# Kernel optimization log

Hardware: AMD Instinct MI355X
Metric: run time of the kernel (lower is better)

## Reference

```python
import jax, jax.numpy as jnp
import numpy as np

HID = 4096; H = 128; P = 64; N = 128; G = 8; K = 4; CH = 128
INTER = H * P                      # 8192
CONV_DIM = INTER + 2 * G * N       # 10240
PROJ = INTER + CONV_DIM + H        # 18560
EPS = 1e-5


def segsum(x):
    # stable segment-sum: out[..., i, j] = sum_{j < k <= i} x[..., k]; -inf above diagonal
    T = x.shape[-1]
    xe = jnp.repeat(x[..., None], T, axis=-1)          # [..., i, j] = x[..., i]
    strict = jnp.tril(jnp.ones((T, T), bool), -1)
    s = jnp.cumsum(jnp.where(strict, xe, 0.0), axis=-2)
    keep = jnp.tril(jnp.ones((T, T), bool), 0)
    return jnp.where(keep, s, -jnp.inf)


def setup_inputs() -> dict:
    key = jax.random.key(0)
    ks = jax.random.split(key, 6)
    b, L = 2, 2048
    hidden_states = jax.random.normal(ks[0], (b, L, HID), jnp.float32)
    in_proj_w = jax.random.normal(ks[1], (PROJ, HID), jnp.float32) * (HID ** -0.5)
    conv_w = jax.random.normal(ks[2], (CONV_DIM, 1, K), jnp.float32) * 0.2
    conv_b = jax.random.normal(ks[3], (CONV_DIM,), jnp.float32) * 0.02
    dt_bias = jnp.ones((H,), jnp.float32)
    A_log = jnp.log(jnp.arange(1, H + 1, dtype=jnp.float32))
    D = jnp.ones((H,), jnp.float32)
    norm_weight = jnp.ones((INTER,), jnp.float32)
    out_proj_w = jax.random.normal(ks[4], (HID, INTER), jnp.float32) * (INTER ** -0.5)
    return dict(hidden_states=hidden_states, in_proj_w=in_proj_w, conv_w=conv_w, conv_b=conv_b,
                dt_bias=dt_bias, A_log=A_log, D=D, norm_weight=norm_weight, out_proj_w=out_proj_w)


def _mamba2(hidden_states, in_proj_w, conv_w, conv_b, dt_bias, A_log, D, norm_weight, out_proj_w):
    b, L, _ = hidden_states.shape
    nchunk = L // CH  # seq_len chosen to be a multiple of chunk_size (pad_size = 0)

    # in_proj and split into gate | conv path (x,B,C) | dt
    proj = hidden_states @ in_proj_w.T
    gate, hBC, dt = jnp.split(proj, [INTER, INTER + CONV_DIM], axis=-1)

    # causal depthwise conv1d (padding k-1, truncate) + SiLU
    xp = jnp.pad(hBC.transpose(0, 2, 1), ((0, 0), (0, 0), (K - 1, 0)))
    xc = jax.lax.conv_general_dilated(xp, conv_w, (1,), 'VALID',
                                      feature_group_count=CONV_DIM,
                                      dimension_numbers=('NCW', 'OIW', 'NCW'))
    hBC = jax.nn.silu((xc + conv_b[None, :, None]).transpose(0, 2, 1))
    hs, Bx, Cx = jnp.split(hBC, [INTER, INTER + G * N], axis=-1)

    A = -jnp.exp(A_log)                      # [H]
    dt = jax.nn.softplus(dt + dt_bias)       # time_step_limit = (0, inf) -> clamp is no-op

    hs = hs.reshape(b, L, H, P)
    rep = H // G
    Bm = jnp.tile(Bx.reshape(b, L, G, N), (1, 1, rep, 1))   # matches torch .repeat
    Cm = jnp.tile(Cx.reshape(b, L, G, N), (1, 1, rep, 1))

    D_res = D[None, None, :, None] * hs      # [b,L,H,P]

    # discretize and chunk
    X = (hs * dt[..., None]).reshape(b, nchunk, CH, H, P)
    A_dt = (A[None, None, :] * dt).reshape(b, nchunk, CH, H).transpose(0, 3, 1, 2)  # [b,H,c,l]
    Bc = Bm.reshape(b, nchunk, CH, H, N)
    Cc = Cm.reshape(b, nchunk, CH, H, N)
    A_cs = jnp.cumsum(A_dt, axis=-1)

    # 1. intra-chunk (diagonal blocks)
    Lmat = jnp.exp(segsum(A_dt))                              # [b,H,c,l,s]
    Gm = jnp.einsum('bclhn,bcshn->bclsh', Cc, Bc)
    M = Gm * Lmat.transpose(0, 2, 3, 4, 1)                    # [b,c,l,s,H]
    Y_diag = jnp.einsum('bclsh,bcshp->bclhp', M, X)

    # 2. per-chunk states
    decay_states = jnp.exp(A_cs[..., -1:] - A_cs)             # [b,H,c,l]
    B_decay = Bc * decay_states.transpose(0, 2, 3, 1)[..., None]
    states = jnp.einsum('bclhn,bclhp->bchpn', B_decay, X)     # [b,c,H,P,N]

    # 3. inter-chunk recurrence
    states = jnp.concatenate([jnp.zeros_like(states[:, :1]), states], axis=1)
    A_last = jnp.pad(A_cs[..., -1], ((0, 0), (0, 0), (1, 0)))  # [b,H,c+1]
    decay_chunk = jnp.exp(segsum(A_last)).transpose(0, 3, 2, 1)  # [b,c+1,c+1,H]
    new_states = jnp.einsum('bzjh,bzhpn->bjhpn', decay_chunk, states)
    prev_states = new_states[:, :-1]                           # [b,c,H,P,N]

    # 4. state -> output
    sdo = jnp.exp(A_cs).transpose(0, 2, 3, 1)                  # [b,c,l,H]
    Y_off = jnp.einsum('bclhn,bchpn->bclhp', Cc, prev_states) * sdo[..., None]

    y = (Y_diag + Y_off).reshape(b, L, H, P) + D_res
    scan_out = y.reshape(b, L, INTER)

    # gated group RMSNorm (norm_before_gate=False: gate first, then group-RMS)
    xg = scan_out * jax.nn.silu(gate)
    xr = xg.reshape(b, L, G, INTER // G)
    xr = xr * jax.lax.rsqrt(jnp.mean(xr * xr, axis=-1, keepdims=True) + EPS)
    normed = xr.reshape(b, L, INTER) * norm_weight

    return normed @ out_proj_w.T


def reference(hidden_states, in_proj_w, conv_w, conv_b, dt_bias, A_log, D, norm_weight, out_proj_w):
    return _mamba2(hidden_states, in_proj_w, conv_w, conv_b, dt_bias, A_log, D, norm_weight, out_proj_w)
```

## Files before the change

### kernel.cpp

```cpp
#include <hip/hip_runtime.h>

#define NH 128
#define PD 64
#define NSD 128
#define NG 8
#define CHK 128
#define HIDD 4096
#define INTER_D 8192
#define CONV_D 10240
#define PROJ_D 18560
#define NPAD 18688
#define SEQ 2048
#define ROWS 4096
#define NCH 16

typedef __attribute__((ext_vector_type(8))) short bf16x8;
typedef __attribute__((ext_vector_type(4))) float f32x4;

__device__ __forceinline__ unsigned short f2bf(float f) {
  unsigned int u = __float_as_uint(f);
  u += 0x7FFF + ((u >> 16) & 1);
  return (unsigned short)(u >> 16);
}
__device__ __forceinline__ float bf2f(unsigned short s) {
  return __uint_as_float(((unsigned int)s) << 16);
}

__device__ __forceinline__ void gld16(const unsigned short* g, unsigned short* l) {
  __builtin_amdgcn_global_load_lds(
      (__attribute__((address_space(1))) const void*)g,
      (__attribute__((address_space(3))) void*)l, 16, 0, 0);
}

#define BAR() __builtin_amdgcn_s_barrier()
#define SCHED() __builtin_amdgcn_sched_barrier(0)
#define VMCNT(n) asm volatile("s_waitcnt vmcnt(" #n ")" ::: "memory")

__device__ __forceinline__ bf16x8 ldsfrag(const unsigned short* slot, int row, int kslot) {
  int byte = row * 128 + (((kslot ^ (row & 7)) << 4));
  return *(const bf16x8*)((const char*)slot + byte);
}

__global__ __launch_bounds__(256) void cvt_kernel(const float* __restrict__ in,
                                                  unsigned short* __restrict__ out,
                                                  size_t n) {
  size_t i = ((size_t)blockIdx.x * 256 + threadIdx.x) * 4;
  if (i < n) {
    float4 f = *(const float4*)(in + i);
    ushort4 o;
    o.x = f2bf(f.x); o.y = f2bf(f.y); o.z = f2bf(f.z); o.w = f2bf(f.w);
    *(ushort4*)(out + i) = o;
  }
}

template <int OUT_BF16>
__global__ __launch_bounds__(512, 2) void gemm256(const unsigned short* __restrict__ A,
                                                  const unsigned short* __restrict__ B,
                                                  unsigned short* __restrict__ outb,
                                                  float* __restrict__ outf,
                                                  int Nreal, int K) {
  __shared__ unsigned short lds[8][8192];
  int tid = threadIdx.x, l = tid & 63, w = tid >> 6;
  int wm = w >> 2, wn = w & 3;
  int il = l & 15, fog = l >> 4;
  int bid = blockIdx.x;
  int xcd = bid & 7, local = bid >> 3;
  int mt = xcd * 2 + (local & 1), nt = local >> 1;
  const unsigned short* Abase = A + (size_t)mt * 256 * K;
  const unsigned short* Bbase = B + (size_t)nt * 256 * K;
  int NT = K >> 6;

  f32x4 acc[2][2][4][2];
#pragma unroll
  for (int a = 0; a < 2; ++a)
#pragma unroll
    for (int b = 0; b < 2; ++b)
#pragma unroll
      for (int m = 0; m < 4; ++m)
#pragma unroll
        for (int n = 0; n < 2; ++n) acc[a][b][m][n] = (f32x4){0.f, 0.f, 0.f, 0.f};

  auto STG = [&](int tt, int ty) {
    int tc = tt < NT ? tt : NT - 1;
    const unsigned short* g = ((ty & 1) ? Bbase : Abase) + (size_t)((ty >> 1) * 128) * K + tc * 64;
    unsigned short* sp = (unsigned short*)lds[(tt & 1) * 4 + ty];
#pragma unroll
    for (int j = 0; j < 2; ++j) {
      int row = (j * 8 + w) * 8 + (l >> 3);
      int scol = ((l & 7) ^ (row & 7)) * 8;
      gld16(g + (size_t)row * K + scol, sp + (j * 8 + w) * 512);
    }
  };

#define LDA(SLOT)                                          \
  _Pragma("unroll") for (int mi = 0; mi < 4; ++mi)         \
  _Pragma("unroll") for (int kk = 0; kk < 2; ++kk)         \
      av[mi][kk] = ldsfrag(SLOT, wm * 64 + mi * 16 + il, kk * 4 + fog);
#define LDB(QN, SLOT)                                      \
  _Pragma("unroll") for (int ni = 0; ni < 2; ++ni)         \
  _Pragma("unroll") for (int kk = 0; kk < 2; ++kk)         \
      bv[QN][ni][kk] = ldsfrag(SLOT, wn * 32 + ni * 16 + il, kk * 4 + fog);
#define MFMA_PH(QM, QN)                                    \
  _Pragma("unroll") for (int mi = 0; mi < 4; ++mi)         \
  _Pragma("unroll") for (int ni = 0; ni < 2; ++ni)         \
  _Pragma("unroll") for (int kk = 0; kk < 2; ++kk)         \
      acc[QM][QN][mi][ni] = __builtin_amdgcn_mfma_f32_16x16x32_bf16( \
          av[mi][kk], bv[QN][ni][kk], acc[QM][QN][mi][ni], 0, 0, 0);

  STG(0, 0); STG(0, 1); STG(0, 3); STG(0, 2);
  VMCNT(2);
  BAR(); SCHED();

  for (int t = 0; t < NT; ++t) {
    const unsigned short* sA0 = lds[(t & 1) * 4 + 0];
    const unsigned short* sB0 = lds[(t & 1) * 4 + 1];
    const unsigned short* sA1 = lds[(t & 1) * 4 + 2];
    const unsigned short* sB1 = lds[(t & 1) * 4 + 3];
    bf16x8 av[4][2], bv[2][2][2];
    LDA(sA0); LDB(0, sB0); LDB(1, sB1);
    STG(t + 1, 0); STG(t + 1, 1);
    BAR();
    __builtin_amdgcn_s_setprio(1);
    MFMA_PH(0, 0);
    __builtin_amdgcn_s_setprio(0);
    VMCNT(4);
    BAR(); SCHED();
    STG(t + 1, 3);
    __builtin_amdgcn_s_setprio(1);
    MFMA_PH(0, 1);
    __builtin_amdgcn_s_setprio(0);
    BAR();
    LDA(sA1);
    STG(t + 1, 2);
    BAR();
    __builtin_amdgcn_s_setprio(1);
    MFMA_PH(1, 0);
    __builtin_amdgcn_s_setprio(0);
    BAR();
    __builtin_amdgcn_s_setprio(1);
    MFMA_PH(1, 1);
    __builtin_amdgcn_s_setprio(0);
    VMCNT(2);
    BAR(); SCHED();
  }

  int rl = (l >> 4) * 4;
#pragma unroll
  for (int qm = 0; qm < 2; ++qm)
#pragma unroll
    for (int qn = 0; qn < 2; ++qn)
#pragma unroll
      for (int mi = 0; mi < 4; ++mi)
#pragma unroll
        for (int ni = 0; ni < 2; ++ni) {
          int grow = mt * 256 + qm * 128 + wm * 64 + mi * 16 + rl;
          int gcol = nt * 256 + qn * 128 + wn * 32 + ni * 16 + il;
          if (!OUT_BF16 || gcol < Nreal) {
#pragma unroll
            for (int r = 0; r < 4; ++r) {
              float v = acc[qm][qn][mi][ni][r];
              if (OUT_BF16)
                outb[(size_t)(grow + r) * Nreal + gcol] = f2bf(v);
              else
                outf[(size_t)(grow + r) * Nreal + gcol] = v;
            }
          }
        }
#undef LDA
#undef LDB
#undef MFMA_PH
}

__global__ __launch_bounds__(128) void dts_kernel(const unsigned short* __restrict__ proj,
                                                  const float* __restrict__ dt_bias,
                                                  const float* __restrict__ A_log,
                                                  float* __restrict__ dtg,
                                                  float* __restrict__ acsg) {
  int bc = blockIdx.x;
  int h = threadIdx.x;
  int b = bc >> 4, c = bc & 15;
  float A = -__expf(A_log[h]);
  float bias = dt_bias[h];
  float cum = 0.f;
  int row0 = b * SEQ + c * CHK;
  for (int ll = 0; ll < CHK; ++ll) {
    float x = bf2f(proj[(size_t)(row0 + ll) * PROJ_D + (PROJ_D - NH) + h]) + bias;
    float d = (x > 20.f) ? x : log1pf(expf(x));
    dtg[(size_t)(row0 + ll) * NH + h] = d;
    cum += A * d;
    acsg[(((size_t)bc * NH) + h) * CHK + ll] = cum;
  }
}

__global__ __launch_bounds__(256) void conv_kernel(const unsigned short* __restrict__ proj,
                                                   const float* __restrict__ cw,
                                                   const float* __restrict__ cb,
                                                   unsigned short* __restrict__ xbc) {
  int ch = blockIdx.x * 256 + threadIdx.x;
  int row = blockIdx.y;
  int b = row >> 11, ll = row & 2047;
  float acc = cb[ch];
#pragma unroll
  for (int k = 0; k < 4; ++k) {
    int l2 = ll - 3 + k;
    if (l2 >= 0)
      acc += bf2f(proj[(size_t)(b * SEQ + l2) * PROJ_D + INTER_D + ch]) * cw[ch * 4 + k];
  }
  float s = acc / (1.f + __expf(-acc));
  xbc[(size_t)row * CONV_D + ch] = f2bf(s);
}

__global__ __launch_bounds__(512) void e1a_kernel(const unsigned short* __restrict__ xbc,
                                                  const float* __restrict__ dtg,
                                                  const float* __restrict__ acsg,
                                                  float* __restrict__ yb) {
  int bid = blockIdx.x;
  int h = bid & 127, c = (bid >> 7) & 15, b = bid >> 11;
  int g = h & 7;
  int row0 = b * SEQ + c * CHK;
  __shared__ __align__(16) char smem[53248];
  unsigned short* Cst = (unsigned short*)smem;
  unsigned short* Bst = (unsigned short*)(smem + 10240);
  unsigned short* Mt = (unsigned short*)smem;
  unsigned short* XT = (unsigned short*)(smem + 34816);
  float* Acs = (float*)(smem + 52224);
  int tid = threadIdx.x, lane = tid & 63, wv = tid >> 6;
  int fo = (lane >> 4) * 8, il = lane & 15, rl = (lane >> 4) * 4;
  if (tid < 128) Acs[tid] = acsg[(((size_t)(b * NCH + c) * NH) + h) * CHK + tid];

  f32x4 gm[8];
#pragma unroll
  for (int i = 0; i < 8; ++i) gm[i] = (f32x4){0.f, 0.f, 0.f, 0.f};
  int srow = tid >> 2, scol = (tid & 3) * 8;
  for (int kc = 0; kc < 4; ++kc) {
    __syncthreads();
    *(int4*)(Cst + srow * 40 + scol) =
        *(const int4*)(xbc + (size_t)(row0 + srow) * CONV_D + INTER_D + NG * NSD + g * NSD + kc * 32 + scol);
    *(int4*)(Bst + srow * 40 + scol) =
        *(const int4*)(xbc + (size_t)(row0 + srow) * CONV_D + INTER_D + g * NSD + kc * 32 + scol);
    __syncthreads();
    bf16x8 a = *(const bf16x8*)&Cst[(wv * 16 + il) * 40 + fo];
#pragma unroll
    for (int ni = 0; ni < 8; ++ni) {
      bf16x8 bb = *(const bf16x8*)&Bst[(ni * 16 + il) * 40 + fo];
      gm[ni] = __builtin_amdgcn_mfma_f32_16x16x32_bf16(a, bb, gm[ni], 0, 0, 0);
    }
  }
  __syncthreads();
#pragma unroll
  for (int ni = 0; ni < 8; ++ni) {
    int s = ni * 16 + il;
#pragma unroll
    for (int r = 0; r < 4; ++r) {
      int ll = wv * 16 + rl + r;
      float v = (s <= ll) ? gm[ni][r] * __expf(Acs[ll] - Acs[s]) : 0.f;
      Mt[ll * 136 + s] = f2bf(v);
    }
  }
#pragma unroll
  for (int j = 0; j < 2; ++j) {
    int q = tid + j * 512;
    int ll = q >> 3, p0 = (q & 7) * 8;
    int row = row0 + ll;
    float dtv = dtg[(size_t)row * NH + h];
    int4 raw = *(const int4*)(xbc + (size_t)row * CONV_D + h * PD + p0);
    unsigned short* u = (unsigned short*)&raw;
#pragma unroll
    for (int e = 0; e < 8; ++e) XT[(p0 + e) * 136 + ll] = f2bf(bf2f(u[e]) * dtv);
  }
  __syncthreads();
  f32x4 yd[4];
#pragma unroll
  for (int i = 0; i < 4; ++i) yd[i] = (f32x4){0.f, 0.f, 0.f, 0.f};
#pragma unroll
  for (int ks = 0; ks < 4; ++ks) {
    bf16x8 a = *(const bf16x8*)&Mt[(wv * 16 + il) * 136 + ks * 32 + fo];
#pragma unroll
    for (int pi = 0; pi < 4; ++pi) {
      bf16x8 bb = *(const bf16x8*)&XT[(pi * 16 + il) * 136 + ks * 32 + fo];
      yd[pi] = __builtin_amdgcn_mfma_f32_16x16x32_bf16(a, bb, yd[pi], 0, 0, 0);
    }
  }
#pragma unroll
  for (int pi = 0; pi < 4; ++pi) {
    int p = pi * 16 + il;
#pragma unroll
    for (int r = 0; r < 4; ++r) {
      int ll = wv * 16 + rl + r;
      yb[(size_t)(row0 + ll) * INTER_D + h * PD + p] = yd[pi][r];
    }
  }
}

__global__ __launch_bounds__(256) void e1b_kernel(const unsigned short* __restrict__ xbc,
                                                  const float* __restrict__ dtg,
                                                  const float* __restrict__ acsg,
                                                  float* __restrict__ states) {
  int bid = blockIdx.x;
  int h = bid & 127, c = (bid >> 7) & 15, b = bid >> 11;
  int g = h & 7;
  int row0 = b * SEQ + c * CHK;
  __shared__ __align__(16) char smem[52736];
  unsigned short* XT = (unsigned short*)smem;
  unsigned short* BdT = (unsigned short*)(smem + 17408);
  float* Acs = (float*)(smem + 52224);
  int tid = threadIdx.x, lane = tid & 63, wv = tid >> 6;
  int fo = (lane >> 4) * 8, il = lane & 15, rl = (lane >> 4) * 4;
  if (tid < 128) Acs[tid] = acsg[(((size_t)(b * NCH + c) * NH) + h) * CHK + tid];
  __syncthreads();
#pragma unroll
  for (int j = 0; j < 4; ++j) {
    int q = tid + j * 256;
    int ll = q >> 3, p0 = (q & 7) * 8;
    int row = row0 + ll;
    float dtv = dtg[(size_t)row * NH + h];
    int4 raw = *(const int4*)(xbc + (size_t)row * CONV_D + h * PD + p0);
    unsigned short* u = (unsigned short*)&raw;
#pragma unroll
    for (int e = 0; e < 8; ++e) XT[(p0 + e) * 136 + ll] = f2bf(bf2f(u[e]) * dtv);
  }
#pragma unroll
  for (int j = 0; j < 8; ++j) {
    int q = tid + j * 256;
    int ll = q >> 4, n0 = (q & 15) * 8;
    float dec = __expf(Acs[CHK - 1] - Acs[ll]);
    int4 raw = *(const int4*)(xbc + (size_t)(row0 + ll) * CONV_D + INTER_D + g * NSD + n0);
    unsigned short* u = (unsigned short*)&raw;
#pragma unroll
    for (int e = 0; e < 8; ++e) BdT[(n0 + e) * 136 + ll] = f2bf(bf2f(u[e]) * dec);
  }
  __syncthreads();
  f32x4 st[8];
#pragma unroll
  for (int i = 0; i < 8; ++i) st[i] = (f32x4){0.f, 0.f, 0.f, 0.f};
#pragma unroll
  for (int ks = 0; ks < 4; ++ks) {
    bf16x8 a = *(const bf16x8*)&XT[(wv * 16 + il) * 136 + ks * 32 + fo];
#pragma unroll
    for (int ni = 0; ni < 8; ++ni) {
      bf16x8 bb = *(const bf16x8*)&BdT[(ni * 16 + il) * 136 + ks * 32 + fo];
      st[ni] = __builtin_amdgcn_mfma_f32_16x16x32_bf16(a, bb, st[ni], 0, 0, 0);
    }
  }
  size_t base = ((size_t)(b * NH + h) * NCH + c) * (PD * NSD);
#pragma unroll
  for (int ni = 0; ni < 8; ++ni) {
    int n = ni * 16 + il;
#pragma unroll
    for (int r = 0; r < 4; ++r) {
      int p = wv * 16 + rl + r;
      states[base + p * NSD + n] = st[ni][r];
    }
  }
}

__global__ __launch_bounds__(256) void e2_kernel(const float* __restrict__ acsg,
                                                 float* __restrict__ states) {
  int bh = blockIdx.x;
  int b = bh >> 7, h = bh & 127;
  int t = threadIdx.x;
  float S[32];
#pragma unroll
  for (int j = 0; j < 32; ++j) S[j] = 0.f;
  for (int c = 0; c < NCH; ++c) {
    float alast = acsg[(((size_t)(b * NCH + c) * NH) + h) * CHK + (CHK - 1)];
    float dec = __expf(alast);
    size_t base = ((size_t)bh * NCH + c) * (PD * NSD);
#pragma unroll
    for (int j = 0; j < 32; ++j) {
      size_t e = base + (size_t)j * 256 + t;
      float v = states[e];
      states[e] = S[j];
      S[j] = S[j] * dec + v;
    }
  }
}

__global__ __launch_bounds__(256) void e3_kernel(const unsigned short* __restrict__ xbc,
                                                 const float* __restrict__ acsg,
                                                 const float* __restrict__ states,
                                                 float* __restrict__ yb) {
  int bid = blockIdx.x;
  int h = bid & 127, c = (bid >> 7) & 15, b = bid >> 11;
  int g = h & 7;
  int row0 = b * SEQ + c * CHK;
  __shared__ __align__(16) char smem[52736];
  unsigned short* Ct = (unsigned short*)smem;
  unsigned short* Sp = (unsigned short*)(smem + 34816);
  float* Acs = (float*)(smem + 52224);
  int tid = threadIdx.x, lane = tid & 63, wv = tid >> 6;
  int fo = (lane >> 4) * 8, il = lane & 15, rl = (lane >> 4) * 4;
  if (tid < 128) Acs[tid] = acsg[(((size_t)(b * NCH + c) * NH) + h) * CHK + tid];
  size_t sbase = ((size_t)(b * NH + h) * NCH + c) * (PD * NSD);
#pragma unroll
  for (int j = 0; j < 8; ++j) {
    int q = tid + j * 256;
    int ll = q >> 4, n0 = (q & 15) * 8;
    *(int4*)(Ct + ll * 136 + n0) =
        *(const int4*)(xbc + (size_t)(row0 + ll) * CONV_D + INTER_D + NG * NSD + g * NSD + n0);
  }
#pragma unroll
  for (int j = 0; j < 4; ++j) {
    int q = tid + j * 256;
    int p = q >> 4, n0 = (q & 15) * 8;
    unsigned short tmp[8];
#pragma unroll
    for (int e = 0; e < 8; ++e) tmp[e] = f2bf(states[sbase + p * NSD + n0 + e]);
    *(int4*)(Sp + p * 136 + n0) = *(int4*)tmp;
  }
  __syncthreads();
  f32x4 yo[2][4];
#pragma unroll
  for (int i = 0; i < 2; ++i)
#pragma unroll
    for (int j = 0; j < 4; ++j) yo[i][j] = (f32x4){0.f, 0.f, 0.f, 0.f};
#pragma unroll
  for (int ks = 0; ks < 4; ++ks) {
    bf16x8 a0 = *(const bf16x8*)&Ct[(wv * 32 + il) * 136 + ks * 32 + fo];
    bf16x8 a1 = *(const bf16x8*)&Ct[(wv * 32 + 16 + il) * 136 + ks * 32 + fo];
#pragma unroll
    for (int pi = 0; pi < 4; ++pi) {
      bf16x8 bb = *(const bf16x8*)&Sp[(pi * 16 + il) * 136 + ks * 32 + fo];
      yo[0][pi] = __builtin_amdgcn_mfma_f32_16x16x32_bf16(a0, bb, yo[0][pi], 0, 0, 0);
      yo[1][pi] = __builtin_amdgcn_mfma_f32_16x16x32_bf16(a1, bb, yo[1][pi], 0, 0, 0);
    }
  }
#pragma unroll
  for (int mi = 0; mi < 2; ++mi)
#pragma unroll
    for (int pi = 0; pi < 4; ++pi)
#pragma unroll
      for (int r = 0; r < 4; ++r) {
        int ll = wv * 32 + mi * 16 + rl + r;
        int p = pi * 16 + il;
        size_t idx = (size_t)(row0 + ll) * INTER_D + h * PD + p;
        yb[idx] += yo[mi][pi][r] * __expf(Acs[ll]);
      }
}

__global__ __launch_bounds__(256) void fnorm_kernel(const float* __restrict__ yb,
                                                    const unsigned short* __restrict__ xbc,
                                                    const unsigned short* __restrict__ proj,
                                                    const float* __restrict__ Dp,
                                                    const float* __restrict__ nw,
                                                    unsigned short* __restrict__ normed) {
  int row = blockIdx.x >> 3;
  int gg = blockIdx.x & 7;
  int t = threadIdx.x;
  float v[4];
  float ss = 0.f;
#pragma unroll
  for (int j = 0; j < 4; ++j) {
    int ch = gg * 1024 + j * 256 + t;
    int h = ch >> 6;
    float yy = yb[(size_t)row * INTER_D + ch];
    float hs = bf2f(xbc[(size_t)row * CONV_D + ch]);
    float gt = bf2f(proj[(size_t)row * PROJ_D + ch]);
    float val = yy + Dp[h] * hs;
    val *= gt / (1.f + __expf(-gt));
    v[j] = val;
    ss += val * val;
  }
  __shared__ float sred[256];
  sred[t] = ss;
  __syncthreads();
  for (int ofs = 128; ofs > 0; ofs >>= 1) {
    if (t < ofs) sred[t] += sred[t + ofs];
    __syncthreads();
  }
  float rms = rsqrtf(sred[0] / 1024.f + 1e-5f);
#pragma unroll
  for (int j = 0; j < 4; ++j) {
    int ch = gg * 1024 + j * 256 + t;
    normed[(size_t)row * INTER_D + ch] = f2bf(v[j] * rms * nw[ch]);
  }
}

extern "C" void kernel_launch(void* const* d_in, const int* in_sizes, int n_in,
                              void* d_out, int out_size, void* d_ws, size_t ws_size,
                              hipStream_t stream) {
  (void)in_sizes; (void)n_in; (void)out_size; (void)ws_size;
  const float* hs = (const float*)d_in[0];
  const float* w1 = (const float*)d_in[1];
  const float* cw = (const float*)d_in[2];
  const float* cb = (const float*)d_in[3];
  const float* dtb = (const float*)d_in[4];
  const float* alog = (const float*)d_in[5];
  const float* Dp = (const float*)d_in[6];
  const float* nw = (const float*)d_in[7];
  const float* w2 = (const float*)d_in[8];
  float* out = (float*)d_out;
  char* ws = (char*)d_ws;

  unsigned short* hsb = (unsigned short*)(ws);
  unsigned short* w1b = (unsigned short*)(ws + 33554432);
  unsigned short* w2b = (unsigned short*)(ws + 186646528);
  unsigned short* proj = (unsigned short*)(ws + 253755392);
  unsigned short* xbc = (unsigned short*)(ws + 405798912);
  float* dtg = (float*)(ws + 489684992);
  float* acsg = (float*)(ws + 491782144);
  float* states = (float*)(ws + 493879296);
  float* yb = (float*)(ws + 628097024);
  unsigned short* normed = (unsigned short*)(ws);

  cvt_kernel<<<dim3(16384), dim3(256), 0, stream>>>(hs, hsb, (size_t)ROWS * HIDD);
  cvt_kernel<<<dim3(74240), dim3(256), 0, stream>>>(w1, w1b, (size_t)PROJ_D * HIDD);
  cvt_kernel<<<dim3(32768), dim3(256), 0, stream>>>(w2, w2b, (size_t)HIDD * INTER_D);

  gemm256<1><<<dim3(16 * 73), dim3(512), 0, stream>>>(hsb, w1b, proj, nullptr,
                                                      PROJ_D, HIDD);
  dts_kernel<<<dim3(32), dim3(128), 0, stream>>>(proj, dtb, alog, dtg, acsg);
  conv_kernel<<<dim3(40, 4096), dim3(256), 0, stream>>>(proj, cw, cb, xbc);
  e1a_kernel<<<dim3(4096), dim3(512), 0, stream>>>(xbc, dtg, acsg, yb);
  e1b_kernel<<<dim3(4096), dim3(256), 0, stream>>>(xbc, dtg, acsg, states);
  e2_kernel<<<dim3(256), dim3(256), 0, stream>>>(acsg, states);
  e3_kernel<<<dim3(4096), dim3(256), 0, stream>>>(xbc, acsg, states, yb);
  fnorm_kernel<<<dim3(32768), dim3(256), 0, stream>>>(yb, xbc, proj, Dp, nw, normed);
  gemm256<0><<<dim3(16 * 16), dim3(512), 0, stream>>>(normed, w2b, nullptr, out,
                                                      HIDD, INTER_D);
}
```

Before: 1.511 ms.

## Fuse intra-chunk and state-output scan kernels, fold D residual, reorder GEMM staging

Merges the diagonal-block (e1a) and off-diagonal state-to-output (e3) kernels into a single e13 kernel, run after the state recurrence, that writes yb once with Y_diag + Y_off + D*x. This removes the yb write-then-read-modify-write round trip and the extra xbc/Dp reads in fnorm. The GEMM main loop now issues all four next-tile global-to-LDS stages up front with a wider vmcnt wait. In exchange, e13 uses more LDS per block (about 69 KB), which may reduce occupancy.

```diff
diff --git a/kernel.cpp b/kernel.cpp
--- a/kernel.cpp
+++ b/kernel.cpp
@@ -9,7 +9,6 @@
 #define INTER_D 8192
 #define CONV_D 10240
 #define PROJ_D 18560
-#define NPAD 18688
 #define SEQ 2048
 #define ROWS 4096
 #define NCH 16
@@ -118,20 +117,18 @@
     const unsigned short* sB1 = lds[(t & 1) * 4 + 3];
     bf16x8 av[4][2], bv[2][2][2];
     LDA(sA0); LDB(0, sB0); LDB(1, sB1);
-    STG(t + 1, 0); STG(t + 1, 1);
+    STG(t + 1, 0); STG(t + 1, 1); STG(t + 1, 3); STG(t + 1, 2);
     BAR();
     __builtin_amdgcn_s_setprio(1);
     MFMA_PH(0, 0);
     __builtin_amdgcn_s_setprio(0);
-    VMCNT(4);
+    VMCNT(8);
     BAR(); SCHED();
-    STG(t + 1, 3);
     __builtin_amdgcn_s_setprio(1);
     MFMA_PH(0, 1);
     __builtin_amdgcn_s_setprio(0);
     BAR();
     LDA(sA1);
-    STG(t + 1, 2);
     BAR();
     __builtin_amdgcn_s_setprio(1);
     MFMA_PH(1, 0);
@@ -210,88 +207,6 @@
   xbc[(size_t)row * CONV_D + ch] = f2bf(s);
 }
 
-__global__ __launch_bounds__(512) void e1a_kernel(const unsigned short* __restrict__ xbc,
-                                                  const float* __restrict__ dtg,
-                                                  const float* __restrict__ acsg,
-                                                  float* __restrict__ yb) {
-  int bid = blockIdx.x;
-  int h = bid & 127, c = (bid >> 7) & 15, b = bid >> 11;
-  int g = h & 7;
-  int row0 = b * SEQ + c * CHK;
-  __shared__ __align__(16) char smem[53248];
-  unsigned short* Cst = (unsigned short*)smem;
-  unsigned short* Bst = (unsigned short*)(smem + 10240);
-  unsigned short* Mt = (unsigned short*)smem;
-  unsigned short* XT = (unsigned short*)(smem + 34816);
-  float* Acs = (float*)(smem + 52224);
-  int tid = threadIdx.x, lane = tid & 63, wv = tid >> 6;
-  int fo = (lane >> 4) * 8, il = lane & 15, rl = (lane >> 4) * 4;
-  if (tid < 128) Acs[tid] = acsg[(((size_t)(b * NCH + c) * NH) + h) * CHK + tid];
-
-  f32x4 gm[8];
-#pragma unroll
-  for (int i = 0; i < 8; ++i) gm[i] = (f32x4){0.f, 0.f, 0.f, 0.f};
-  int srow = tid >> 2, scol = (tid & 3) * 8;
-  for (int kc = 0; kc < 4; ++kc) {
-    __syncthreads();
-    *(int4*)(Cst + srow * 40 + scol) =
-        *(const int4*)(xbc + (size_t)(row0 + srow) * CONV_D + INTER_D + NG * NSD + g * NSD + kc * 32 + scol);
-    *(int4*)(Bst + srow * 40 + scol) =
-        *(const int4*)(xbc + (size_t)(row0 + srow) * CONV_D + INTER_D + g * NSD + kc * 32 + scol);
-    __syncthreads();
-    bf16x8 a = *(const bf16x8*)&Cst[(wv * 16 + il) * 40 + fo];
-#pragma unroll
-    for (int ni = 0; ni < 8; ++ni) {
-      bf16x8 bb = *(const bf16x8*)&Bst[(ni * 16 + il) * 40 + fo];
-      gm[ni] = __builtin_amdgcn_mfma_f32_16x16x32_bf16(a, bb, gm[ni], 0, 0, 0);
-    }
-  }
-  __syncthreads();
-#pragma unroll
-  for (int ni = 0; ni < 8; ++ni) {
-    int s = ni * 16 + il;
-#pragma unroll
-    for (int r = 0; r < 4; ++r) {
-      int ll = wv * 16 + rl + r;
-      float v = (s <= ll) ? gm[ni][r] * __expf(Acs[ll] - Acs[s]) : 0.f;
-      Mt[ll * 136 + s] = f2bf(v);
-    }
-  }
-#pragma unroll
-  for (int j = 0; j < 2; ++j) {
-    int q = tid + j * 512;
-    int ll = q >> 3, p0 = (q & 7) * 8;
-    int row = row0 + ll;
-    float dtv = dtg[(size_t)row * NH + h];
-    int4 raw = *(const int4*)(xbc + (size_t)row * CONV_D + h * PD + p0);
-    unsigned short* u = (unsigned short*)&raw;
-#pragma unroll
-    for (int e = 0; e < 8; ++e) XT[(p0 + e) * 136 + ll] = f2bf(bf2f(u[e]) * dtv);
-  }
-  __syncthreads();
-  f32x4 yd[4];
-#pragma unroll
-  for (int i = 0; i < 4; ++i) yd[i] = (f32x4){0.f, 0.f, 0.f, 0.f};
-#pragma unroll
-  for (int ks = 0; ks < 4; ++ks) {
-    bf16x8 a = *(const bf16x8*)&Mt[(wv * 16 + il) * 136 + ks * 32 + fo];
-#pragma unroll
-    for (int pi = 0; pi < 4; ++pi) {
-      bf16x8 bb = *(const bf16x8*)&XT[(pi * 16 + il) * 136 + ks * 32 + fo];
-      yd[pi] = __builtin_amdgcn_mfma_f32_16x16x32_bf16(a, bb, yd[pi], 0, 0, 0);
-    }
-  }
-#pragma unroll
-  for (int pi = 0; pi < 4; ++pi) {
-    int p = pi * 16 + il;
-#pragma unroll
-    for (int r = 0; r < 4; ++r) {
-      int ll = wv * 16 + rl + r;
-      yb[(size_t)(row0 + ll) * INTER_D + h * PD + p] = yd[pi][r];
-    }
-  }
-}
-
 __global__ __launch_bounds__(256) void e1b_kernel(const unsigned short* __restrict__ xbc,
                                                   const float* __restrict__ dtg,
                                                   const float* __restrict__ acsg,
@@ -376,72 +291,129 @@
   }
 }
 
-__global__ __launch_bounds__(256) void e3_kernel(const unsigned short* __restrict__ xbc,
-                                                 const float* __restrict__ acsg,
-                                                 const float* __restrict__ states,
-                                                 float* __restrict__ yb) {
+__global__ __launch_bounds__(512) void e13_kernel(const unsigned short* __restrict__ xbc,
+                                                  const float* __restrict__ dtg,
+                                                  const float* __restrict__ acsg,
+                                                  const float* __restrict__ states,
+                                                  const float* __restrict__ Dp,
+                                                  float* __restrict__ yb) {
   int bid = blockIdx.x;
   int h = bid & 127, c = (bid >> 7) & 15, b = bid >> 11;
   int g = h & 7;
   int row0 = b * SEQ + c * CHK;
-  __shared__ __align__(16) char smem[52736];
+  __shared__ __align__(16) char smem[70144];
+  unsigned short* Cst = (unsigned short*)smem;
+  unsigned short* Bst = (unsigned short*)(smem + 10240);
+  unsigned short* Mt = (unsigned short*)smem;
   unsigned short* Ct = (unsigned short*)smem;
-  unsigned short* Sp = (unsigned short*)(smem + 34816);
-  float* Acs = (float*)(smem + 52224);
+  unsigned short* XT = (unsigned short*)(smem + 34816);
+  unsigned short* Sp = (unsigned short*)(smem + 52224);
+  float* Acs = (float*)(smem + 69632);
   int tid = threadIdx.x, lane = tid & 63, wv = tid >> 6;
   int fo = (lane >> 4) * 8, il = lane & 15, rl = (lane >> 4) * 4;
   if (tid < 128) Acs[tid] = acsg[(((size_t)(b * NCH + c) * NH) + h) * CHK + tid];
+
+  f32x4 gm[8];
+#pragma unroll
+  for (int i = 0; i < 8; ++i) gm[i] = (f32x4){0.f, 0.f, 0.f, 0.f};
+  int srow = tid >> 2, scol = (tid & 3) * 8;
+  for (int kc = 0; kc < 4; ++kc) {
+    __syncthreads();
+    *(int4*)(Cst + srow * 40 + scol) =
+        *(const int4*)(xbc + (size_t)(row0 + srow) * CONV_D + INTER_D + NG * NSD + g * NSD + kc * 32 + scol);
+    *(int4*)(Bst + srow * 40 + scol) =
+        *(const int4*)(xbc + (size_t)(row0 + srow) * CONV_D + INTER_D + g * NSD + kc * 32 + scol);
+    __syncthreads();
+    bf16x8 a = *(const bf16x8*)&Cst[(wv * 16 + il) * 40 + fo];
+#pragma unroll
+    for (int ni = 0; ni < 8; ++ni) {
+      bf16x8 bb = *(const bf16x8*)&Bst[(ni * 16 + il) * 40 + fo];
+      gm[ni] = __builtin_amdgcn_mfma_f32_16x16x32_bf16(a, bb, gm[ni], 0, 0, 0);
+    }
+  }
+  __syncthreads();
+#pragma unroll
+  for (int ni = 0; ni < 8; ++ni) {
+    int s = ni * 16 + il;
+#pragma unroll
+    for (int r = 0; r < 4; ++r) {
+      int ll = wv * 16 + rl + r;
+      float v = (s <= ll) ? gm[ni][r] * __expf(Acs[ll] - Acs[s]) : 0.f;
+      Mt[ll * 136 + s] = f2bf(v);
+    }
+  }
+#pragma unroll
+  for (int j = 0; j < 2; ++j) {
+    int q = tid + j * 512;
+    int ll = q >> 3, p0 = (q & 7) * 8;
+    int row = row0 + ll;
+    float dtv = dtg[(size_t)row * NH + h];
+    int4 raw = *(const int4*)(xbc + (size_t)row * CONV_D + h * PD + p0);
+    unsigned short* u = (unsigned short*)&raw;
+#pragma unroll
+    for (int e = 0; e < 8; ++e) XT[(p0 + e) * 136 + ll] = f2bf(bf2f(u[e]) * dtv);
+  }
   size_t sbase = ((size_t)(b * NH + h) * NCH + c) * (PD * NSD);
 #pragma unroll
-  for (int j = 0; j < 8; ++j) {
-    int q = tid + j * 256;
+  for (int j = 0; j < 2; ++j) {
+    int q = tid + j * 512;
+    int p = q >> 4, n0 = (q & 15) * 8;
+    unsigned short tmp[8];
+#pragma unroll
+    for (int e = 0; e < 8; ++e) tmp[e] = f2bf(states[sbase + p * NSD + n0 + e]);
+    *(int4*)(Sp + p * 136 + n0) = *(int4*)tmp;
+  }
+  __syncthreads();
+  f32x4 yd[4];
+#pragma unroll
+  for (int i = 0; i < 4; ++i) yd[i] = (f32x4){0.f, 0.f, 0.f, 0.f};
+#pragma unroll
+  for (int ks = 0; ks < 4; ++ks) {
+    bf16x8 a = *(const bf16x8*)&Mt[(wv * 16 + il) * 136 + ks * 32 + fo];
+#pragma unroll
+    for (int pi = 0; pi < 4; ++pi) {
+      bf16x8 bb = *(const bf16x8*)&XT[(pi * 16 + il) * 136 + ks * 32 + fo];
+      yd[pi] = __builtin_amdgcn_mfma_f32_16x16x32_bf16(a, bb, yd[pi], 0, 0, 0);
+    }
+  }
+  __syncthreads();
+#pragma unroll
+  for (int j = 0; j < 4; ++j) {
+    int q = tid + j * 512;
     int ll = q >> 4, n0 = (q & 15) * 8;
     *(int4*)(Ct + ll * 136 + n0) =
         *(const int4*)(xbc + (size_t)(row0 + ll) * CONV_D + INTER_D + NG * NSD + g * NSD + n0);
   }
-#pragma unroll
-  for (int j = 0; j < 4; ++j) {
-    int q = tid + j * 256;
-    int p = q >> 4, n0 = (q & 15) * 8;
-    unsigned short tmp[8];
-#pragma unroll
-    for (int e = 0; e < 8; ++e) tmp[e] = f2bf(states[sbase + p * NSD + n0 + e]);
-    *(int4*)(Sp + p * 136 + n0) = *(int4*)tmp;
-  }
-  __syncthreads();
-  f32x4 yo[2][4];
-#pragma unroll
-  for (int i = 0; i < 2; ++i)
-#pragma unroll
-    for (int j = 0; j < 4; ++j) yo[i][j] = (f32x4){0.f, 0.f, 0.f, 0.f};
+  __syncthreads();
+  f32x4 yo[4];
+#pragma unroll
+  for (int i = 0; i < 4; ++i) yo[i] = (f32x4){0.f, 0.f, 0.f, 0.f};
 #pragma unroll
   for (int ks = 0; ks < 4; ++ks) {
-    bf16x8 a0 = *(const bf16x8*)&Ct[(wv * 32 + il) * 136 + ks * 32 + fo];
-    bf16x8 a1 = *(const bf16x8*)&Ct[(wv * 32 + 16 + il) * 136 + ks * 32 + fo];
+    bf16x8 a = *(const bf16x8*)&Ct[(wv * 16 + il) * 136 + ks * 32 + fo];
 #pragma unroll
     for (int pi = 0; pi < 4; ++pi) {
       bf16x8 bb = *(const bf16x8*)&Sp[(pi * 16 + il) * 136 + ks * 32 + fo];
-      yo[0][pi] = __builtin_amdgcn_mfma_f32_16x16x32_bf16(a0, bb, yo[0][pi], 0, 0, 0);
-      yo[1][pi] = __builtin_amdgcn_mfma_f32_16x16x32_bf16(a1, bb, yo[1][pi], 0, 0, 0);
-    }
-  }
-#pragma unroll
-  for (int mi = 0; mi < 2; ++mi)
-#pragma unroll
-    for (int pi = 0; pi < 4; ++pi)
-#pragma unroll
-      for (int r = 0; r < 4; ++r) {
-        int ll = wv * 32 + mi * 16 + rl + r;
-        int p = pi * 16 + il;
-        size_t idx = (size_t)(row0 + ll) * INTER_D + h * PD + p;
-        yb[idx] += yo[mi][pi][r] * __expf(Acs[ll]);
-      }
+      yo[pi] = __builtin_amdgcn_mfma_f32_16x16x32_bf16(a, bb, yo[pi], 0, 0, 0);
+    }
+  }
+  float dv = Dp[h];
+#pragma unroll
+  for (int pi = 0; pi < 4; ++pi) {
+    int p = pi * 16 + il;
+#pragma unroll
+    for (int r = 0; r < 4; ++r) {
+      int ll = wv * 16 + rl + r;
+      int row = row0 + ll;
+      float hsv = bf2f(xbc[(size_t)row * CONV_D + h * PD + p]);
+      yb[(size_t)row * INTER_D + h * PD + p] =
+          yd[pi][r] + yo[pi][r] * __expf(Acs[ll]) + dv * hsv;
+    }
+  }
 }
 
 __global__ __launch_bounds__(256) void fnorm_kernel(const float* __restrict__ yb,
-                                                    const unsigned short* __restrict__ xbc,
                                                     const unsigned short* __restrict__ proj,
-                                                    const float* __restrict__ Dp,
                                                     const float* __restrict__ nw,
                                                     unsigned short* __restrict__ normed) {
   int row = blockIdx.x >> 3;
@@ -452,11 +424,8 @@
 #pragma unroll
   for (int j = 0; j < 4; ++j) {
     int ch = gg * 1024 + j * 256 + t;
-    int h = ch >> 6;
-    float yy = yb[(size_t)row * INTER_D + ch];
-    float hs = bf2f(xbc[(size_t)row * CONV_D + ch]);
+    float val = yb[(size_t)row * INTER_D + ch];
     float gt = bf2f(proj[(size_t)row * PROJ_D + ch]);
-    float val = yy + Dp[h] * hs;
     val *= gt / (1.f + __expf(-gt));
     v[j] = val;
     ss += val * val;
@@ -511,11 +480,10 @@
                                                       PROJ_D, HIDD);
   dts_kernel<<<dim3(32), dim3(128), 0, stream>>>(proj, dtb, alog, dtg, acsg);
   conv_kernel<<<dim3(40, 4096), dim3(256), 0, stream>>>(proj, cw, cb, xbc);
-  e1a_kernel<<<dim3(4096), dim3(512), 0, stream>>>(xbc, dtg, acsg, yb);
   e1b_kernel<<<dim3(4096), dim3(256), 0, stream>>>(xbc, dtg, acsg, states);
   e2_kernel<<<dim3(256), dim3(256), 0, stream>>>(acsg, states);
-  e3_kernel<<<dim3(4096), dim3(256), 0, stream>>>(xbc, acsg, states, yb);
-  fnorm_kernel<<<dim3(32768), dim3(256), 0, stream>>>(yb, xbc, proj, Dp, nw, normed);
+  e13_kernel<<<dim3(4096), dim3(512), 0, stream>>>(xbc, dtg, acsg, states, Dp, yb);
+  fnorm_kernel<<<dim3(32768), dim3(256), 0, stream>>>(yb, proj, nw, normed);
   gemm256<0><<<dim3(16 * 16), dim3(512), 0, stream>>>(normed, w2b, nullptr, out,
                                                       HIDD, INTER_D);
 }
```

After: 1.573 ms. 1.04x slower.
